# Kernel tuning notes

Measured on AMD Instinct MI355X. Metric: run time of the kernel, lower is better.

Reference implementation:

```python
import jax, jax.numpy as jnp
import numpy as np

B = 131072      # batch of states
N_ACT = 40      # output_dim (Tetris action space)


def setup_inputs() -> dict:
    key = jax.random.key(0)
    ks = jax.random.split(key, 9)
    # state vector: 11 real-valued board features, 1 hold-piece id in [0,4),
    # 3 next-piece ids in [1,8) (0 is treated as invalid by the original code)
    keep = jax.random.normal(ks[0], (B, 11), dtype=jnp.float32)
    hold = jax.random.randint(ks[1], (B, 1), 0, 4).astype(jnp.float32)
    nxt = jax.random.randint(ks[2], (B, 3), 1, 8).astype(jnp.float32)
    x = jnp.concatenate([keep, hold, nxt], axis=1)  # [B, 15]
    W1 = jax.random.normal(ks[3], (36, 128), dtype=jnp.float32) * 0.1
    b1 = jnp.zeros((128,), dtype=jnp.float32)
    W2 = jax.random.normal(ks[4], (128, 512), dtype=jnp.float32) * 0.05
    b2 = jnp.zeros((512,), dtype=jnp.float32)
    W4 = jax.random.normal(ks[5], (512, N_ACT), dtype=jnp.float32) * 0.05
    b4 = jnp.zeros((N_ACT,), dtype=jnp.float32)
    return {"x": x, "W1": W1, "b1": b1, "W2": W2, "b2": b2, "W4": W4, "b4": b4}


def reference(x, W1, b1, W2, b2, W4, b4):
    B_, _ = x.shape
    keep = x[:, :11]                                      # [B, 11]
    # vectorized replacement of the per-sample .item() one-hot loop
    hold_idx = jax.lax.stop_gradient(jnp.clip(x[:, 11].astype(jnp.int32), 0, 3))
    nxt_idx = jax.lax.stop_gradient(jnp.clip(x[:, 12:15].astype(jnp.int32) - 1, 0, 6))
    hold_oh = jax.nn.one_hot(hold_idx, 4, dtype=x.dtype)  # [B, 4]
    nxt_oh = jax.nn.one_hot(nxt_idx, 7, dtype=x.dtype).reshape(B_, 21)  # [B, 21]
    inp = jnp.concatenate([keep, hold_oh, nxt_oh], axis=1)  # [B, 36]
    h = jax.nn.relu(inp @ W1 + b1)   # [B, 128]
    h = jax.nn.relu(h @ W2 + b2)     # [B, 512]
    return h @ W4 + b4               # [B, N_ACT]
```

## Files before the change

### kernel.cpp

```cpp
#include <hip/hip_runtime.h>


typedef short bf16x8 __attribute__((ext_vector_type(8)));
typedef float f32x4 __attribute__((ext_vector_type(4)));
typedef unsigned int u32;

#define NW1F 8192
#define NW2F 65536
#define NW4F 24576
#define PACK_TOTAL (NW1F + NW2F + NW4F)
#define PACK_THREADS (PACK_TOTAL / 8)

__device__ __forceinline__ unsigned short f2bf(float f) {
  union { float f; unsigned u; } a; a.f = f;
  unsigned r = a.u + 0x7fffu + ((a.u >> 16) & 1u);
  return (unsigned short)(r >> 16);
}
__device__ __forceinline__ u32 cvtpk(float lo, float hi) {
  u32 r;
  asm("v_cvt_pk_bf16_f32 %0, %1, %2" : "=v"(r) : "v"(lo), "v"(hi));
  return r;
}

__global__ void pack_weights(const float* __restrict__ W1,
                             const float* __restrict__ W2,
                             const float* __restrict__ W4,
                             unsigned short* __restrict__ wf) {
  int t = blockIdx.x * 256 + threadIdx.x;
  if (t >= PACK_THREADS) return;
  int fid = t >> 6, lane = t & 63;
  int l16 = lane & 15, quad = lane >> 4;
  float vals[8];
  if (fid < 16) {
    int mt = fid >> 1, ks = fid & 1;
    int m = mt * 16 + l16, k0 = ks * 32 + quad * 8;
#pragma unroll
    for (int j = 0; j < 8; ++j) { int k = k0 + j; vals[j] = (k < 36) ? W1[k * 128 + m] : 0.f; }
  } else if (fid < 144) {
    int f = fid - 16, mt = f >> 2, ks = f & 3;
    int m = mt * 16 + l16, k0 = ks * 32 + quad * 8;
#pragma unroll
    for (int j = 0; j < 8; ++j) vals[j] = W2[(k0 + j) * 512 + m];
  } else {
    int f = fid - 144, mt = f >> 4, ks = f & 15;
    int m = mt * 16 + l16, k0 = ks * 32 + quad * 8;
#pragma unroll
    for (int j = 0; j < 8; ++j) vals[j] = (m < 40) ? W4[(k0 + j) * 40 + m] : 0.f;
  }
  u32 p[4];
#pragma unroll
  for (int j = 0; j < 4; ++j) p[j] = cvtpk(vals[2 * j], vals[2 * j + 1]);
  *(bf16x8*)(wf + (size_t)t * 8) = *(bf16x8*)p;
}

__global__ __launch_bounds__(128, 2) void dqn_fused(
    const float* __restrict__ x,
    const unsigned short* __restrict__ wf,
    const float* __restrict__ b1,
    const float* __restrict__ b2,
    const float* __restrict__ b4,
    float* __restrict__ out) {
  __shared__ __align__(16) unsigned short sBuf[2 * 64 * 72];

  const int tid  = threadIdx.x;
  const int lane = tid & 63;
  const int wave = tid >> 6;
  const int quad = lane >> 4;
  const int l16  = lane & 15;
  const int row0 = blockIdx.x << 7;
  const int lr0  = wave * 64;
  unsigned short* su = sBuf + wave * (64 * 72);

  const unsigned short* w2f = wf + NW1F;
  const unsigned short* w4f = wf + NW1F + NW2F;
  const unsigned short* w2p = w2f + lane * 8;

  bf16x8 W[2][4];
#pragma unroll
  for (int k = 0; k < 4; ++k) W[0][k] = *(const bf16x8*)(w2p + (size_t)k * 512);

  {
    const float* xr = x + (size_t)(row0 + lr0 + lane) * 15;
    unsigned short* dst = su + lane * 72;
    bf16x8 z = {0, 0, 0, 0, 0, 0, 0, 0};
#pragma unroll
    for (int c = 8; c < 64; c += 8) *(bf16x8*)(dst + c) = z;
    u32 p[4];
#pragma unroll
    for (int i = 0; i < 4; ++i) p[i] = cvtpk(xr[2 * i], xr[2 * i + 1]);
    *(bf16x8*)dst = *(bf16x8*)p;
    *(u32*)(dst + 8) = cvtpk(xr[8], xr[9]);
    dst[10] = f2bf(xr[10]);
    int hold = (int)xr[11]; hold = hold < 0 ? 0 : (hold > 3 ? 3 : hold);
    dst[11 + hold] = 0x3F80;
#pragma unroll
    for (int t = 0; t < 3; ++t) {
      int nx = (int)xr[12 + t] - 1; nx = nx < 0 ? 0 : (nx > 6 ? 6 : nx);
      dst[15 + t * 7 + nx] = 0x3F80;
    }
  }

  const f32x4 vzero = {0.f, 0.f, 0.f, 0.f};

  bf16x8 ib[4][2];
#pragma unroll
  for (int rg = 0; rg < 4; ++rg)
#pragma unroll
    for (int ks = 0; ks < 2; ++ks)
      ib[rg][ks] = *(const bf16x8*)(su + (rg * 16 + l16) * 72 + ks * 32 + quad * 8);

  bf16x8 af1[4][4];
#pragma unroll
  for (int half = 0; half < 2; ++half) {
    bf16x8 wa[4][2];
#pragma unroll
    for (int mtl = 0; mtl < 4; ++mtl)
#pragma unroll
      for (int ks = 0; ks < 2; ++ks)
        wa[mtl][ks] = *(const bf16x8*)(
            wf + (size_t)(((half * 4 + mtl) * 2 + ks) * 64 + lane) * 8);

    f32x4 acc1[4][4];
#pragma unroll
    for (int mtl = 0; mtl < 4; ++mtl)
#pragma unroll
      for (int rg = 0; rg < 4; ++rg) acc1[mtl][rg] = vzero;

    __builtin_amdgcn_s_setprio(1);
#pragma unroll
    for (int mtl = 0; mtl < 4; ++mtl)
#pragma unroll
      for (int ks = 0; ks < 2; ++ks)
#pragma unroll
        for (int rg = 0; rg < 4; ++rg)
          acc1[mtl][rg] = __builtin_amdgcn_mfma_f32_16x16x32_bf16(wa[mtl][ks], ib[rg][ks], acc1[mtl][rg], 0, 0, 0);
    __builtin_amdgcn_s_setprio(0);

#pragma unroll
    for (int mtl = 0; mtl < 4; ++mtl) {
      f32x4 bias = *(const f32x4*)(b1 + (half * 4 + mtl) * 16 + quad * 4);
#pragma unroll
      for (int rg = 0; rg < 4; ++rg) {
        float v0 = fmaxf(acc1[mtl][rg][0] + bias[0], 0.f);
        float v1 = fmaxf(acc1[mtl][rg][1] + bias[1], 0.f);
        float v2 = fmaxf(acc1[mtl][rg][2] + bias[2], 0.f);
        float v3 = fmaxf(acc1[mtl][rg][3] + bias[3], 0.f);
        uint2 pk = {cvtpk(v0, v1), cvtpk(v2, v3)};
        *(uint2*)(su + (rg * 16 + l16) * 72 + mtl * 16 + quad * 4) = pk;
      }
    }
#pragma unroll
    for (int rg = 0; rg < 4; ++rg)
#pragma unroll
      for (int ksl = 0; ksl < 2; ++ksl)
        af1[rg][half * 2 + ksl] =
            *(const bf16x8*)(su + (rg * 16 + l16) * 72 + ksl * 32 + quad * 8);
  }

  f32x4 accO[3][4];
#pragma unroll
  for (int mt = 0; mt < 3; ++mt)
#pragma unroll
    for (int rg = 0; rg < 4; ++rg) accO[mt][rg] = vzero;

  for (int chunk = 0; chunk < 8; ++chunk) {
    f32x4 bias2[4];
#pragma unroll
    for (int mtl = 0; mtl < 4; ++mtl)
      bias2[mtl] = *(const f32x4*)(b2 + chunk * 64 + mtl * 16 + quad * 4);

#pragma unroll
    for (int mtl = 0; mtl < 4; ++mtl) {
      int fb = chunk * 16 + mtl * 4 + 4;
      if (fb >= 128) fb = 0;
#pragma unroll
      for (int k = 0; k < 4; ++k)
        W[(mtl + 1) & 1][k] = *(const bf16x8*)(w2p + (size_t)(fb + k) * 512);

      f32x4 acc2[4];
#pragma unroll
      for (int rg = 0; rg < 4; ++rg) acc2[rg] = bias2[mtl];

      __builtin_amdgcn_s_setprio(1);
#pragma unroll
      for (int ks = 0; ks < 4; ++ks)
#pragma unroll
        for (int rg = 0; rg < 4; ++rg)
          acc2[rg] = __builtin_amdgcn_mfma_f32_16x16x32_bf16(W[mtl & 1][ks], af1[rg][ks], acc2[rg], 0, 0, 0);
      __builtin_amdgcn_s_setprio(0);

#pragma unroll
      for (int rg = 0; rg < 4; ++rg) {
        float v0 = fmaxf(acc2[rg][0], 0.f);
        float v1 = fmaxf(acc2[rg][1], 0.f);
        float v2 = fmaxf(acc2[rg][2], 0.f);
        float v3 = fmaxf(acc2[rg][3], 0.f);
        uint2 pk = {cvtpk(v0, v1), cvtpk(v2, v3)};
        *(uint2*)(su + (rg * 16 + l16) * 72 + mtl * 16 + quad * 4) = pk;
      }
    }

#pragma unroll
    for (int ks3 = 0; ks3 < 2; ++ks3) {
      bf16x8 w4r[3];
#pragma unroll
      for (int mt3 = 0; mt3 < 3; ++mt3)
        w4r[mt3] = *(const bf16x8*)(
            w4f + (size_t)((mt3 * 16 + chunk * 2 + ks3) * 64 + lane) * 8);
      bf16x8 h[4];
#pragma unroll
      for (int rg = 0; rg < 4; ++rg)
        h[rg] = *(const bf16x8*)(su + (rg * 16 + l16) * 72 + ks3 * 32 + quad * 8);
      __builtin_amdgcn_s_setprio(1);
#pragma unroll
      for (int mt3 = 0; mt3 < 3; ++mt3)
#pragma unroll
        for (int rg = 0; rg < 4; ++rg)
          accO[mt3][rg] = __builtin_amdgcn_mfma_f32_16x16x32_bf16(w4r[mt3], h[rg], accO[mt3][rg], 0, 0, 0);
      __builtin_amdgcn_s_setprio(0);
    }
  }

#pragma unroll
  for (int mt3 = 0; mt3 < 3; ++mt3) {
    int colbase = mt3 * 16 + quad * 4;
    if (colbase < 40) {
      f32x4 bias = *(const f32x4*)(b4 + colbase);
#pragma unroll
      for (int rg = 0; rg < 4; ++rg) {
        f32x4 v = accO[mt3][rg] + bias;
        size_t row = (size_t)(row0 + lr0 + rg * 16 + l16);
        *(f32x4*)(out + row * 40 + colbase) = v;
      }
    }
  }
}

extern "C" void kernel_launch(void* const* d_in, const int* in_sizes, int n_in,
                              void* d_out, int out_size, void* d_ws, size_t ws_size,
                              hipStream_t stream) {
  const float* x  = (const float*)d_in[0];
  const float* W1 = (const float*)d_in[1];
  const float* b1 = (const float*)d_in[2];
  const float* W2 = (const float*)d_in[3];
  const float* b2 = (const float*)d_in[4];
  const float* W4 = (const float*)d_in[5];
  const float* b4 = (const float*)d_in[6];
  float* out = (float*)d_out;
  unsigned short* wf = (unsigned short*)d_ws;

  int B = in_sizes[0] / 15;

  hipLaunchKernelGGL(pack_weights, dim3((PACK_THREADS + 255) / 256), dim3(256), 0, stream,
                     W1, W2, W4, wf);
  hipLaunchKernelGGL(dqn_fused, dim3(B / 128), dim3(128), 0, stream,
                     x, wf, b1, b2, b4, out);
}
```

Baseline: 97.52 us.

## Double-buffer hidden layer in LDS and software-pipeline layer-3 MFMAs behind layer-2

Widens the per-row LDS stride to hold two 64-column halves of the layer-2 activation so chunk c can be written while chunk c-1 is read. Layer-3 MFMAs for the previous chunk are interleaved between layer-2 MFMA steps of the current chunk, with a prologue and epilogue, so the MFMA pipe has independent work while waiting on LDS round trips. The layer-1 bias is also folded into the accumulator initialisation instead of being added after the MFMA. The cost is a larger LDS footprint and more live registers, which could reduce occupancy or cause spills.

```diff
diff --git a/kernel.cpp b/kernel.cpp
--- a/kernel.cpp
+++ b/kernel.cpp
@@ -10,6 +10,8 @@
 #define NW4F 24576
 #define PACK_TOTAL (NW1F + NW2F + NW4F)
 #define PACK_THREADS (PACK_TOTAL / 8)
+
+#define SROW 136
 
 __device__ __forceinline__ unsigned short f2bf(float f) {
   union { float f; unsigned u; } a; a.f = f;
@@ -53,6 +55,56 @@
   *(bf16x8*)(wf + (size_t)t * 8) = *(bf16x8*)p;
 }
 
+#define MTL_STEP(chunk, mtl, hb)                                               \
+  {                                                                            \
+    int fb = (chunk) * 16 + (mtl) * 4 + 4;                                     \
+    if (fb >= 128) fb = 0;           \
+    _Pragma("unroll")                                                          \
+    for (int k = 0; k < 4; ++k)                                                \
+      W[((mtl) + 1) & 1][k] = *(const bf16x8*)(w2p + (size_t)(fb + k) * 512);  \
+    f32x4 acc2[4];                                                             \
+    _Pragma("unroll")                                                          \
+    for (int rg = 0; rg < 4; ++rg) acc2[rg] = bias2[mtl];                      \
+    __builtin_amdgcn_s_setprio(1);                                             \
+    _Pragma("unroll")                                                          \
+    for (int ks = 0; ks < 4; ++ks)                                             \
+      _Pragma("unroll")                                                        \
+      for (int rg = 0; rg < 4; ++rg)                                           \
+        acc2[rg] = __builtin_amdgcn_mfma_f32_16x16x32_bf16(                    \
+            W[(mtl) & 1][ks], af1[rg][ks], acc2[rg], 0, 0, 0);                 \
+    __builtin_amdgcn_s_setprio(0);                                             \
+    _Pragma("unroll")                                                          \
+    for (int rg = 0; rg < 4; ++rg) {                                           \
+      float v0 = fmaxf(acc2[rg][0], 0.f);                                      \
+      float v1 = fmaxf(acc2[rg][1], 0.f);                                      \
+      float v2 = fmaxf(acc2[rg][2], 0.f);                                      \
+      float v3 = fmaxf(acc2[rg][3], 0.f);                                      \
+      uint2 pk = {cvtpk(v0, v1), cvtpk(v2, v3)};                               \
+      *(uint2*)(su + (rg * 16 + l16) * SROW + (hb) + (mtl) * 16 + quad * 4) = pk; \
+    }                                                                          \
+  }
+
+#define H_READ(dst, hbp, ks3)                                                  \
+  _Pragma("unroll")                                                            \
+  for (int rg = 0; rg < 4; ++rg)                                               \
+    dst[rg] = *(const bf16x8*)(su + (rg * 16 + l16) * SROW + (hbp) + (ks3) * 32 + quad * 8);
+
+#define W4_LOAD(dst, chunkprev, ks3)                                           \
+  _Pragma("unroll")                                                            \
+  for (int mt3 = 0; mt3 < 3; ++mt3)                                            \
+    dst[mt3] = *(const bf16x8*)(                                               \
+        w4f + (size_t)((mt3 * 16 + (chunkprev) * 2 + (ks3)) * 64 + lane) * 8);
+
+#define L3_PART(w4q, hq)                                                       \
+  __builtin_amdgcn_s_setprio(1);                                               \
+  _Pragma("unroll")                                                            \
+  for (int mt3 = 0; mt3 < 3; ++mt3)                                            \
+    _Pragma("unroll")                                                          \
+    for (int rg = 0; rg < 4; ++rg)                                             \
+      accO[mt3][rg] = __builtin_amdgcn_mfma_f32_16x16x32_bf16(                 \
+          w4q[mt3], hq[rg], accO[mt3][rg], 0, 0, 0);                           \
+  __builtin_amdgcn_s_setprio(0);
+
 __global__ __launch_bounds__(128, 2) void dqn_fused(
     const float* __restrict__ x,
     const unsigned short* __restrict__ wf,
@@ -60,7 +112,7 @@
     const float* __restrict__ b2,
     const float* __restrict__ b4,
     float* __restrict__ out) {
-  __shared__ __align__(16) unsigned short sBuf[2 * 64 * 72];
+  __shared__ __align__(16) unsigned short sBuf[2 * 64 * SROW];
 
   const int tid  = threadIdx.x;
   const int lane = tid & 63;
@@ -69,7 +121,7 @@
   const int l16  = lane & 15;
   const int row0 = blockIdx.x << 7;
   const int lr0  = wave * 64;
-  unsigned short* su = sBuf + wave * (64 * 72);
+  unsigned short* su = sBuf + wave * (64 * SROW);
 
   const unsigned short* w2f = wf + NW1F;
   const unsigned short* w4f = wf + NW1F + NW2F;
@@ -81,7 +133,7 @@
 
   {
     const float* xr = x + (size_t)(row0 + lr0 + lane) * 15;
-    unsigned short* dst = su + lane * 72;
+    unsigned short* dst = su + lane * SROW;
     bf16x8 z = {0, 0, 0, 0, 0, 0, 0, 0};
 #pragma unroll
     for (int c = 8; c < 64; c += 8) *(bf16x8*)(dst + c) = z;
@@ -107,7 +159,7 @@
   for (int rg = 0; rg < 4; ++rg)
 #pragma unroll
     for (int ks = 0; ks < 2; ++ks)
-      ib[rg][ks] = *(const bf16x8*)(su + (rg * 16 + l16) * 72 + ks * 32 + quad * 8);
+      ib[rg][ks] = *(const bf16x8*)(su + (rg * 16 + l16) * SROW + ks * 32 + quad * 8);
 
   bf16x8 af1[4][4];
 #pragma unroll
@@ -122,9 +174,11 @@
 
     f32x4 acc1[4][4];
 #pragma unroll
-    for (int mtl = 0; mtl < 4; ++mtl)
-#pragma unroll
-      for (int rg = 0; rg < 4; ++rg) acc1[mtl][rg] = vzero;
+    for (int mtl = 0; mtl < 4; ++mtl) {
+      f32x4 bias = *(const f32x4*)(b1 + (half * 4 + mtl) * 16 + quad * 4);
+#pragma unroll
+      for (int rg = 0; rg < 4; ++rg) acc1[mtl][rg] = bias;
+    }
 
     __builtin_amdgcn_s_setprio(1);
 #pragma unroll
@@ -138,15 +192,14 @@
 
 #pragma unroll
     for (int mtl = 0; mtl < 4; ++mtl) {
-      f32x4 bias = *(const f32x4*)(b1 + (half * 4 + mtl) * 16 + quad * 4);
 #pragma unroll
       for (int rg = 0; rg < 4; ++rg) {
-        float v0 = fmaxf(acc1[mtl][rg][0] + bias[0], 0.f);
-        float v1 = fmaxf(acc1[mtl][rg][1] + bias[1], 0.f);
-        float v2 = fmaxf(acc1[mtl][rg][2] + bias[2], 0.f);
-        float v3 = fmaxf(acc1[mtl][rg][3] + bias[3], 0.f);
+        float v0 = fmaxf(acc1[mtl][rg][0], 0.f);
+        float v1 = fmaxf(acc1[mtl][rg][1], 0.f);
+        float v2 = fmaxf(acc1[mtl][rg][2], 0.f);
+        float v3 = fmaxf(acc1[mtl][rg][3], 0.f);
         uint2 pk = {cvtpk(v0, v1), cvtpk(v2, v3)};
-        *(uint2*)(su + (rg * 16 + l16) * 72 + mtl * 16 + quad * 4) = pk;
+        *(uint2*)(su + (rg * 16 + l16) * SROW + mtl * 16 + quad * 4) = pk;
       }
     }
 #pragma unroll
@@ -154,7 +207,7 @@
 #pragma unroll
       for (int ksl = 0; ksl < 2; ++ksl)
         af1[rg][half * 2 + ksl] =
-            *(const bf16x8*)(su + (rg * 16 + l16) * 72 + ksl * 32 + quad * 8);
+            *(const bf16x8*)(su + (rg * 16 + l16) * SROW + ksl * 32 + quad * 8);
   }
 
   f32x4 accO[3][4];
@@ -163,62 +216,50 @@
 #pragma unroll
     for (int rg = 0; rg < 4; ++rg) accO[mt][rg] = vzero;
 
-  for (int chunk = 0; chunk < 8; ++chunk) {
+  {
     f32x4 bias2[4];
 #pragma unroll
     for (int mtl = 0; mtl < 4; ++mtl)
+      bias2[mtl] = *(const f32x4*)(b2 + mtl * 16 + quad * 4);
+    MTL_STEP(0, 0, 0)
+    MTL_STEP(0, 1, 0)
+    MTL_STEP(0, 2, 0)
+    MTL_STEP(0, 3, 0)
+  }
+  for (int chunk = 1; chunk < 8; ++chunk) {
+    const int hb  = (chunk & 1) * 72;
+    const int hbp = 72 - hb;
+    f32x4 bias2[4];
+#pragma unroll
+    for (int mtl = 0; mtl < 4; ++mtl)
       bias2[mtl] = *(const f32x4*)(b2 + chunk * 64 + mtl * 16 + quad * 4);
 
-#pragma unroll
-    for (int mtl = 0; mtl < 4; ++mtl) {
-      int fb = chunk * 16 + mtl * 4 + 4;
-      if (fb >= 128) fb = 0;
-#pragma unroll
-      for (int k = 0; k < 4; ++k)
-        W[(mtl + 1) & 1][k] = *(const bf16x8*)(w2p + (size_t)(fb + k) * 512);
-
-      f32x4 acc2[4];
-#pragma unroll
-      for (int rg = 0; rg < 4; ++rg) acc2[rg] = bias2[mtl];
-
-      __builtin_amdgcn_s_setprio(1);
-#pragma unroll
-      for (int ks = 0; ks < 4; ++ks)
-#pragma unroll
-        for (int rg = 0; rg < 4; ++rg)
-          acc2[rg] = __builtin_amdgcn_mfma_f32_16x16x32_bf16(W[mtl & 1][ks], af1[rg][ks], acc2[rg], 0, 0, 0);
-      __builtin_amdgcn_s_setprio(0);
-
-#pragma unroll
-      for (int rg = 0; rg < 4; ++rg) {
-        float v0 = fmaxf(acc2[rg][0], 0.f);
-        float v1 = fmaxf(acc2[rg][1], 0.f);
-        float v2 = fmaxf(acc2[rg][2], 0.f);
-        float v3 = fmaxf(acc2[rg][3], 0.f);
-        uint2 pk = {cvtpk(v0, v1), cvtpk(v2, v3)};
-        *(uint2*)(su + (rg * 16 + l16) * 72 + mtl * 16 + quad * 4) = pk;
-      }
-    }
-
-#pragma unroll
-    for (int ks3 = 0; ks3 < 2; ++ks3) {
-      bf16x8 w4r[3];
-#pragma unroll
-      for (int mt3 = 0; mt3 < 3; ++mt3)
-        w4r[mt3] = *(const bf16x8*)(
-            w4f + (size_t)((mt3 * 16 + chunk * 2 + ks3) * 64 + lane) * 8);
-      bf16x8 h[4];
-#pragma unroll
-      for (int rg = 0; rg < 4; ++rg)
-        h[rg] = *(const bf16x8*)(su + (rg * 16 + l16) * 72 + ks3 * 32 + quad * 8);
-      __builtin_amdgcn_s_setprio(1);
-#pragma unroll
-      for (int mt3 = 0; mt3 < 3; ++mt3)
-#pragma unroll
-        for (int rg = 0; rg < 4; ++rg)
-          accO[mt3][rg] = __builtin_amdgcn_mfma_f32_16x16x32_bf16(w4r[mt3], h[rg], accO[mt3][rg], 0, 0, 0);
-      __builtin_amdgcn_s_setprio(0);
-    }
+    bf16x8 w4a[3];
+    W4_LOAD(w4a, chunk - 1, 0)
+    MTL_STEP(chunk, 0, hb)
+    bf16x8 h0[4];
+    H_READ(h0, hbp, 0)
+    MTL_STEP(chunk, 1, hb)
+    L3_PART(w4a, h0)
+    bf16x8 w4b[3];
+    W4_LOAD(w4b, chunk - 1, 1)
+    MTL_STEP(chunk, 2, hb)
+    bf16x8 h1v[4];
+    H_READ(h1v, hbp, 1)
+    MTL_STEP(chunk, 3, hb)
+    L3_PART(w4b, h1v)
+  }
+  {
+    bf16x8 w4a[3];
+    W4_LOAD(w4a, 7, 0)
+    bf16x8 h0[4];
+    H_READ(h0, 72, 0)
+    L3_PART(w4a, h0)
+    bf16x8 w4b[3];
+    W4_LOAD(w4b, 7, 1)
+    bf16x8 h1v[4];
+    H_READ(h1v, 72, 1)
+    L3_PART(w4b, h1v)
   }
 
 #pragma unroll
```

New measurement: 96.62 us. About the same (-0.9%).
